# Performance work log

Measured on AMD Instinct MI355X. Metric: run time of the kernel, lower is better.

## Reference

```python
import jax, jax.numpy as jnp
import numpy as np

D_MODEL = 1024
NUM_HEADS = 16
HEAD_DIM = D_MODEL // NUM_HEADS


def setup_inputs() -> dict:
    key = jax.random.key(0)
    ks = jax.random.split(key, 10)
    B, SQ, SKV = 4, 2048, 2048
    s = 1.0 / np.sqrt(D_MODEL)
    return {
        "query": jax.random.normal(ks[0], (B, SQ, D_MODEL), jnp.float32),
        "key_value": jax.random.normal(ks[1], (B, SKV, D_MODEL), jnp.float32),
        "Wq": jax.random.normal(ks[2], (D_MODEL, D_MODEL), jnp.float32) * s,
        "bq": jnp.zeros((D_MODEL,), jnp.float32),
        "Wk": jax.random.normal(ks[3], (D_MODEL, D_MODEL), jnp.float32) * s,
        "bk": jnp.zeros((D_MODEL,), jnp.float32),
        "Wv": jax.random.normal(ks[4], (D_MODEL, D_MODEL), jnp.float32) * s,
        "bv": jnp.zeros((D_MODEL,), jnp.float32),
        "Wo": jax.random.normal(ks[5], (D_MODEL, D_MODEL), jnp.float32) * s,
        "bo": jnp.zeros((D_MODEL,), jnp.float32),
    }


def reference(query, key_value, Wq, bq, Wk, bk, Wv, bv, Wo, bo):
    B, SQ, _ = query.shape
    SKV = key_value.shape[1]
    H, Dh = NUM_HEADS, HEAD_DIM
    # projections (torch Linear: x @ W.T + b); split heads -> (B, H, S, Dh)
    Q = (query @ Wq.T + bq).reshape(B, SQ, H, Dh).transpose(0, 2, 1, 3)
    K = (key_value @ Wk.T + bk).reshape(B, SKV, H, Dh).transpose(0, 2, 1, 3)
    V = (key_value @ Wv.T + bv).reshape(B, SKV, H, Dh).transpose(0, 2, 1, 3)
    scale = jnp.asarray(np.sqrt(Dh), query.dtype)
    scores = jnp.einsum("bhqd,bhkd->bhqk", Q, K) / scale
    weights = jax.nn.softmax(scores, axis=-1)  # dropout is identity in eval
    attn = jnp.einsum("bhqk,bhkd->bhqd", weights, V)
    attn = attn.transpose(0, 2, 1, 3).reshape(B, SQ, H * Dh)
    return attn @ Wo.T + bo
```

## Files before the change

### kernel.cpp

```cpp
#include <hip/hip_runtime.h>

#define NH 16
#define DH 64
#define DM 1024
#define SEQ 2048
#define BATCH 4

typedef short s16x8 __attribute__((ext_vector_type(8)));
typedef float f32x4 __attribute__((ext_vector_type(4)));

__device__ __forceinline__ unsigned short f2bf(float f) {
  union { float f; unsigned int u; } v; v.f = f;
  unsigned int u = v.u;
  unsigned int r = (u + 0x7fffu + ((u >> 16) & 1u)) >> 16;
  return (unsigned short)r;
}

__device__ __forceinline__ unsigned int pkbf(float a, float b) {
#if __has_builtin(__builtin_amdgcn_cvt_pk_bf16_f32)
  typedef short v2s __attribute__((ext_vector_type(2)));
  v2s r = __builtin_amdgcn_cvt_pk_bf16_f32(a, b);
  union { v2s v; unsigned int u; } cv; cv.v = r;
  return cv.u;
#else
  return (unsigned int)f2bf(a) | ((unsigned int)f2bf(b) << 16);
#endif
}

__device__ __forceinline__ float fexp2(float x) {
#if __has_builtin(__builtin_amdgcn_exp2f)
  return __builtin_amdgcn_exp2f(x);
#else
  return exp2f(x);
#endif
}

__device__ __forceinline__ void gload_lds16(const void* g, void* l) {
  __builtin_amdgcn_global_load_lds(
      (const __attribute__((address_space(1))) unsigned int*)g,
      (__attribute__((address_space(3))) unsigned int*)l, 16, 0, 0);
}

__global__ void convert_all(const float* __restrict__ q, const float* __restrict__ kv,
                            const float* __restrict__ w0, const float* __restrict__ w1,
                            const float* __restrict__ w2, const float* __restrict__ w3,
                            unsigned short* __restrict__ oq, unsigned short* __restrict__ okv,
                            unsigned short* __restrict__ ow0, unsigned short* __restrict__ ow1,
                            unsigned short* __restrict__ ow2, unsigned short* __restrict__ ow3) {
  const int NQ4 = (BATCH * SEQ * DM) / 4;
  const int NW4 = (DM * DM) / 4;
  const int total = NQ4 * 2 + NW4 * 4;
  for (int i = blockIdx.x * blockDim.x + threadIdx.x; i < total;
       i += gridDim.x * blockDim.x) {
    const float* s; unsigned short* d; int off;
    if (i < NQ4)            { s = q;  d = oq;  off = i; }
    else if (i < 2 * NQ4)   { s = kv; d = okv; off = i - NQ4; }
    else {
      int j = i - 2 * NQ4; int wsel = j / NW4; off = j - wsel * NW4;
      s = (wsel == 0) ? w0 : (wsel == 1) ? w1 : (wsel == 2) ? w2 : w3;
      d = (wsel == 0) ? ow0 : (wsel == 1) ? ow1 : (wsel == 2) ? ow2 : ow3;
    }
    float4 v = *(const float4*)(s + (size_t)off * 4);
    ushort4 o;
    o.x = f2bf(v.x); o.y = f2bf(v.y); o.z = f2bf(v.z); o.w = f2bf(v.w);
    *(ushort4*)(d + (size_t)off * 4) = o;
  }
}

__device__ __forceinline__ void gemm_tile(const unsigned short* __restrict__ X,
                                          const unsigned short* __restrict__ Wt,
                                          unsigned short* As, unsigned short* Bs,
                                          int m0, int n0, f32x4 (*acc)[4]) {
  const int tid = threadIdx.x;
  const int wv_ = tid >> 6, lane = tid & 63;
  const int quad = lane >> 4, c = lane & 15;
  const int wm = (wv_ >> 1) * 64, wn = (wv_ & 1) * 64;
  const int srow = lane >> 3;
  const int scol = ((lane & 7) ^ srow) * 8;

  for (int kt = 0; kt < DM; kt += 64) {
#pragma unroll
    for (int i = 0; i < 4; ++i) {
      int reg = wv_ * 4 + i;
      gload_lds16(X + (size_t)(m0 + reg * 8 + srow) * DM + kt + scol,
                  (void*)(As + reg * 512));
      gload_lds16(Wt + (size_t)(n0 + reg * 8 + srow) * DM + kt + scol,
                  (void*)(Bs + reg * 512));
    }
    __syncthreads();
#pragma unroll
    for (int k2 = 0; k2 < 2; ++k2) {
      s16x8 a[4], b[4];
      int g = k2 * 4 + quad;
#pragma unroll
      for (int t = 0; t < 4; ++t)
        a[t] = *(const s16x8*)(As + (wm + t * 16 + c) * 64 + ((g ^ (c & 7)) * 8));
#pragma unroll
      for (int t = 0; t < 4; ++t)
        b[t] = *(const s16x8*)(Bs + (wn + t * 16 + c) * 64 + ((g ^ (c & 7)) * 8));
#pragma unroll
      for (int tm = 0; tm < 4; ++tm)
#pragma unroll
        for (int tn = 0; tn < 4; ++tn)
          acc[tm][tn] = __builtin_amdgcn_mfma_f32_16x16x32_bf16(
              a[tm], b[tn], acc[tm][tn], 0, 0, 0);
    }
    __syncthreads();
  }
}

__global__ __launch_bounds__(256)
void gemm_qkv(const unsigned short* __restrict__ Xq,
              const unsigned short* __restrict__ Xkv,
              const unsigned short* __restrict__ W0,
              const unsigned short* __restrict__ W1,
              const unsigned short* __restrict__ W2,
              const float* __restrict__ b0, const float* __restrict__ b1,
              const float* __restrict__ b2,
              unsigned short* __restrict__ OQ, unsigned short* __restrict__ OK_,
              unsigned short* __restrict__ OV) {
  __shared__ alignas(16) unsigned short As[128 * 64];
  __shared__ alignas(16) unsigned short Bs[128 * 64];
  const int m0 = blockIdx.x * 128;
  const int ysel = blockIdx.y >> 3;
  const int n0 = (blockIdx.y & 7) * 128;
  const unsigned short* X = (ysel == 0) ? Xq : Xkv;
  const unsigned short* Wt = (ysel == 0) ? W0 : (ysel == 1) ? W1 : W2;
  const float* bias = (ysel == 0) ? b0 : (ysel == 1) ? b1 : b2;
  unsigned short* Out = (ysel == 0) ? OQ : (ysel == 1) ? OK_ : OV;
  const float scale = (ysel == 0) ? 0.1803368801f : 1.0f;

  f32x4 acc[4][4] = {};
  gemm_tile(X, Wt, As, Bs, m0, n0, acc);

  const int tid = threadIdx.x;
  const int wv_ = tid >> 6, lane = tid & 63;
  const int quad = lane >> 4, c = lane & 15;
  const int wm = (wv_ >> 1) * 64, wn = (wv_ & 1) * 64;
#pragma unroll
  for (int tm = 0; tm < 4; ++tm) {
#pragma unroll
    for (int tn = 0; tn < 4; ++tn) {
      int n = n0 + wn + tn * 16 + c;
      float bv = bias[n];
      int m_base = m0 + wm + tm * 16 + quad * 4;
      if (ysel == 2) {
        int b_ = m_base >> 11, s_ = m_base & 2047, h_ = n >> 6, dh = n & 63;
        size_t idx = (((size_t)(b_ * NH + h_)) * DH + dh) * SEQ + s_;
        ushort4 o4;
        o4.x = f2bf(acc[tm][tn][0] + bv);
        o4.y = f2bf(acc[tm][tn][1] + bv);
        o4.z = f2bf(acc[tm][tn][2] + bv);
        o4.w = f2bf(acc[tm][tn][3] + bv);
        *(ushort4*)(&Out[idx]) = o4;
      } else {
#pragma unroll
        for (int p = 0; p < 4; ++p) {
          int m = m_base + p;
          float val = (acc[tm][tn][p] + bv) * scale;
          int b_ = m >> 11, s_ = m & 2047, h_ = n >> 6, dh = n & 63;
          size_t idx = (((size_t)(b_ * NH + h_)) * SEQ + s_) * DH + dh;
          Out[idx] = f2bf(val);
        }
      }
    }
  }
}

__global__ __launch_bounds__(256)
void gemm_o(const unsigned short* __restrict__ X,
            const unsigned short* __restrict__ Wt,
            const float* __restrict__ bias, float* __restrict__ Out) {
  __shared__ alignas(16) unsigned short As[128 * 64];
  __shared__ alignas(16) unsigned short Bs[128 * 64];
  const int m0 = blockIdx.x * 128;
  const int n0 = blockIdx.y * 128;
  f32x4 acc[4][4] = {};
  gemm_tile(X, Wt, As, Bs, m0, n0, acc);

  const int tid = threadIdx.x;
  const int wv_ = tid >> 6, lane = tid & 63;
  const int quad = lane >> 4, c = lane & 15;
  const int wm = (wv_ >> 1) * 64, wn = (wv_ & 1) * 64;
#pragma unroll
  for (int tm = 0; tm < 4; ++tm) {
#pragma unroll
    for (int tn = 0; tn < 4; ++tn) {
      int n = n0 + wn + tn * 16 + c;
      float bv = bias[n];
#pragma unroll
      for (int p = 0; p < 4; ++p) {
        int m = m0 + wm + tm * 16 + quad * 4 + p;
        Out[(size_t)m * DM + n] = acc[tm][tn][p] + bv;
      }
    }
  }
}

__global__ __launch_bounds__(512, 2)
void attn_kernel(const unsigned short* __restrict__ Qb,
                 const unsigned short* __restrict__ Kb,
                 const unsigned short* __restrict__ VTb,
                 unsigned short* __restrict__ Ob) {
  __shared__ alignas(16) unsigned short SM[18432];

  const int tid = threadIdx.x, wv_ = tid >> 6, lane = tid & 63;
  const int quad = lane >> 4, c = lane & 15;
  const int wg = blockIdx.x;
  const int bh = (wg & 7) + 8 * ((wg >> 3) >> 2);
  const int qb = (wg >> 3) & 3;
  const unsigned short* Qp = Qb + (size_t)bh * SEQ * DH;
  const unsigned short* Kp = Kb + (size_t)bh * SEQ * DH;
  const unsigned short* Vp = VTb + (size_t)bh * DH * SEQ;
  const int wq0 = qb * 512 + wv_ * 64;

  s16x8 aq[4][2];
#pragma unroll
  for (int t = 0; t < 4; ++t)
#pragma unroll
    for (int k2 = 0; k2 < 2; ++k2)
      aq[t][k2] = *(const s16x8*)(Qp + (size_t)(wq0 + t * 16 + c) * DH +
                                  k2 * 32 + quad * 8);

  f32x4 ot[4][4] = {};
  f32x4 lacc[4] = {};
  s16x8 ones;
  {
    union { s16x8 v; unsigned short u[8]; } o_;
#pragma unroll
    for (int j = 0; j < 8; ++j) o_.u[j] = 0x3F80;
    ones = o_.v;
  }

  const int srow = lane >> 3;
  const int sbase = (lane & 7) ^ (srow & 3);

  const int fK = (c & 3) | (((c >> 2) & 1) << 2);
  const int fV = (c & 3) | (((c >> 3) & 1) << 2);

#pragma unroll
  for (int i = 0; i < 2; ++i) {
    int slab = wv_ * 2 + i;
    if (slab < 8) {
      int ch = sbase ^ ((slab & 1) << 2);
      gload_lds16(Kp + (size_t)(slab * 8 + srow) * DH + ch * 8,
                  (void*)(SM + slab * 512));
    } else {
      int s2 = slab - 8;
      int ch = sbase ^ ((s2 & 1) << 2);
      gload_lds16(Vp + (size_t)(s2 * 8 + srow) * SEQ + ch * 8,
                  (void*)(SM + 8192 + s2 * 512));
    }
  }

  for (int kt = 0; kt < SEQ; kt += 64) {
    const int cur = (kt >> 6) & 1;
    __syncthreads();
    if (kt + 64 < SEQ) {
      const int nxt = cur ^ 1;
#pragma unroll
      for (int i = 0; i < 2; ++i) {
        int slab = wv_ * 2 + i;
        if (slab < 8) {
          int ch = sbase ^ ((slab & 1) << 2);
          gload_lds16(Kp + (size_t)(kt + 64 + slab * 8 + srow) * DH + ch * 8,
                      (void*)(SM + nxt * 4096 + slab * 512));
        } else {
          int s2 = slab - 8;
          int ch = sbase ^ ((s2 & 1) << 2);
          gload_lds16(Vp + (size_t)(s2 * 8 + srow) * SEQ + kt + 64 + ch * 8,
                      (void*)(SM + 8192 + nxt * 4096 + s2 * 512));
        }
      }
    }
    const unsigned short* K_ = SM + cur * 4096;
    const unsigned short* V_ = SM + 8192 + cur * 4096;

    f32x4 s[4][2][2] = {};
#pragma unroll
    for (int k2 = 0; k2 < 2; ++k2) {
      s16x8 ak[2][2];
#pragma unroll
      for (int jp = 0; jp < 2; ++jp)
#pragma unroll
        for (int h = 0; h < 2; ++h) {
          int r = jp * 32 + ((c >> 2) << 3) + h * 4 + (c & 3);
          int g = k2 * 4 + quad;
          ak[jp][h] = *(const s16x8*)(K_ + r * 64 + ((g ^ fK) * 8));
        }
#pragma unroll
      for (int t = 0; t < 4; ++t)
#pragma unroll
        for (int jp = 0; jp < 2; ++jp)
#pragma unroll
          for (int h = 0; h < 2; ++h)
            s[t][jp][h] = __builtin_amdgcn_mfma_f32_16x16x32_bf16(
                ak[jp][h], aq[t][k2], s[t][jp][h], 0, 0, 0);
    }

    s16x8 bp[4][2];
#pragma unroll
    for (int t = 0; t < 4; ++t)
#pragma unroll
      for (int jp = 0; jp < 2; ++jp) {
        float e00 = fexp2(s[t][jp][0][0]);
        float e01 = fexp2(s[t][jp][0][1]);
        float e02 = fexp2(s[t][jp][0][2]);
        float e03 = fexp2(s[t][jp][0][3]);
        float e10 = fexp2(s[t][jp][1][0]);
        float e11 = fexp2(s[t][jp][1][1]);
        float e12 = fexp2(s[t][jp][1][2]);
        float e13 = fexp2(s[t][jp][1][3]);
        union { s16x8 v; unsigned int u[4]; } pk;
        pk.u[0] = pkbf(e00, e01);
        pk.u[1] = pkbf(e02, e03);
        pk.u[2] = pkbf(e10, e11);
        pk.u[3] = pkbf(e12, e13);
        bp[t][jp] = pk.v;
        lacc[t] = __builtin_amdgcn_mfma_f32_16x16x32_bf16(
            ones, bp[t][jp], lacc[t], 0, 0, 0);
      }

#pragma unroll
    for (int jp = 0; jp < 2; ++jp)
#pragma unroll
      for (int dt = 0; dt < 4; ++dt) {
        int g = jp * 4 + quad;
        int r = dt * 16 + c;
        s16x8 av = *(const s16x8*)(V_ + r * 64 + ((g ^ fV) * 8));
#pragma unroll
        for (int t = 0; t < 4; ++t)
          ot[dt][t] = __builtin_amdgcn_mfma_f32_16x16x32_bf16(
              av, bp[t][jp], ot[dt][t], 0, 0, 0);
      }
  }

  __syncthreads();

  const int b_ = bh >> 4, h_ = bh & 15;
  const int ql = lane >> 1, hf = lane & 1;
  unsigned short* Lq = SM + wv_ * (32 * 72);
#pragma unroll
  for (int half = 0; half < 2; ++half) {
    if (half) asm volatile("s_waitcnt lgkmcnt(0)" ::: "memory");
#pragma unroll
    for (int t2 = 0; t2 < 2; ++t2) {
      int t = half * 2 + t2;
      float inv = 1.0f / lacc[t][0];
#pragma unroll
      for (int dt = 0; dt < 4; ++dt) {
        unsigned int w01 = pkbf(ot[dt][t][0] * inv, ot[dt][t][1] * inv);
        unsigned int w23 = pkbf(ot[dt][t][2] * inv, ot[dt][t][3] * inv);
        unsigned short* p = Lq + (t2 * 16 + c) * 72 + dt * 16 + quad * 4;
        *(unsigned int*)(p) = w01;
        *(unsigned int*)(p + 2) = w23;
      }
    }
    const unsigned short* Lr = Lq + ql * 72 + hf * 32;
    unsigned short* Og = Ob + ((size_t)(b_ * SEQ + wq0 + half * 32 + ql)) * DM +
                         h_ * 64 + hf * 32;
#pragma unroll
    for (int j = 0; j < 4; ++j) {
      s16x8 v = *(const s16x8*)(Lr + j * 8);
      *(s16x8*)(Og + j * 8) = v;
    }
  }
}

extern "C" void kernel_launch(void* const* d_in, const int* in_sizes, int n_in,
                              void* d_out, int out_size, void* d_ws, size_t ws_size,
                              hipStream_t stream) {
  const float* q  = (const float*)d_in[0];
  const float* kv = (const float*)d_in[1];
  const float* Wq = (const float*)d_in[2];
  const float* bq = (const float*)d_in[3];
  const float* Wk = (const float*)d_in[4];
  const float* bk = (const float*)d_in[5];
  const float* Wv = (const float*)d_in[6];
  const float* bv = (const float*)d_in[7];
  const float* Wo = (const float*)d_in[8];
  const float* bo = (const float*)d_in[9];

  char* ws = (char*)d_ws;
  const size_t MB = 1024 * 1024;
  unsigned short* q_bf  = (unsigned short*)(ws);
  unsigned short* kv_bf = (unsigned short*)(ws + 16 * MB);
  unsigned short* wq_bf = (unsigned short*)(ws + 32 * MB);
  unsigned short* wk_bf = (unsigned short*)(ws + 34 * MB);
  unsigned short* wv_bf = (unsigned short*)(ws + 36 * MB);
  unsigned short* wo_bf = (unsigned short*)(ws + 38 * MB);
  unsigned short* Qb    = (unsigned short*)(ws + 40 * MB);
  unsigned short* Kb    = (unsigned short*)(ws + 56 * MB);
  unsigned short* VTb   = (unsigned short*)(ws + 72 * MB);
  unsigned short* attn  = (unsigned short*)(ws + 88 * MB);

  convert_all<<<2048, 256, 0, stream>>>(q, kv, Wq, Wk, Wv, Wo,
                                        q_bf, kv_bf, wq_bf, wk_bf, wv_bf, wo_bf);
  gemm_qkv<<<dim3(64, 24), 256, 0, stream>>>(q_bf, kv_bf, wq_bf, wk_bf, wv_bf,
                                             bq, bk, bv, Qb, Kb, VTb);
  attn_kernel<<<dim3(256), 512, 0, stream>>>(Qb, Kb, VTb, attn);
  gemm_o<<<dim3(64, 8), 256, 0, stream>>>(attn, wo_bf, bo, (float*)d_out);
}
```

Baseline: 305.4 us.

## Stage 128-key tiles per barrier and raise MFMA wave priority in attention

The attention loop now stages K and V tiles of 128 keys per double-buffered step instead of 64, which halves the number of block barriers and makes each wave issue four async global-to-LDS loads per step. Each stage is processed as two 64-key halves. MFMA bursts are also wrapped in s_setprio so matrix work is favoured over other waves. Shared memory grows from about 36KB to 64KB per block, which could limit two blocks per CU under the launch bounds.

```diff
diff --git a/kernel.cpp b/kernel.cpp
--- a/kernel.cpp
+++ b/kernel.cpp
@@ -202,7 +202,7 @@
                  const unsigned short* __restrict__ Kb,
                  const unsigned short* __restrict__ VTb,
                  unsigned short* __restrict__ Ob) {
-  __shared__ alignas(16) unsigned short SM[18432];
+  __shared__ alignas(16) unsigned short SM[32768];
 
   const int tid = threadIdx.x, wv_ = tid >> 6, lane = tid & 63;
   const int quad = lane >> 4, c = lane & 15;
@@ -233,106 +233,97 @@
   }
 
   const int srow = lane >> 3;
-  const int sbase = (lane & 7) ^ (srow & 3);
+  const int ch = ((lane & 7) ^ (srow & 3)) ^ ((wv_ & 1) << 2);
 
   const int fK = (c & 3) | (((c >> 2) & 1) << 2);
   const int fV = (c & 3) | (((c >> 3) & 1) << 2);
 
-#pragma unroll
-  for (int i = 0; i < 2; ++i) {
-    int slab = wv_ * 2 + i;
-    if (slab < 8) {
-      int ch = sbase ^ ((slab & 1) << 2);
-      gload_lds16(Kp + (size_t)(slab * 8 + srow) * DH + ch * 8,
-                  (void*)(SM + slab * 512));
-    } else {
-      int s2 = slab - 8;
-      int ch = sbase ^ ((s2 & 1) << 2);
-      gload_lds16(Vp + (size_t)(s2 * 8 + srow) * SEQ + ch * 8,
-                  (void*)(SM + 8192 + s2 * 512));
-    }
-  }
-
-  for (int kt = 0; kt < SEQ; kt += 64) {
-    const int cur = (kt >> 6) & 1;
+#define STAGE_TILE(ktt, buf)                                                   \
+  {                                                                            \
+    gload_lds16(Kp + (size_t)((ktt) + wv_ * 8 + srow) * DH + ch * 8,           \
+                (void*)(SM + (buf) * 8192 + wv_ * 512));                       \
+    gload_lds16(Kp + (size_t)((ktt) + 64 + wv_ * 8 + srow) * DH + ch * 8,      \
+                (void*)(SM + (buf) * 8192 + 4096 + wv_ * 512));                \
+    gload_lds16(Vp + (size_t)(wv_ * 8 + srow) * SEQ + (ktt) + ch * 8,          \
+                (void*)(SM + 16384 + (buf) * 8192 + wv_ * 512));               \
+    gload_lds16(Vp + (size_t)(wv_ * 8 + srow) * SEQ + (ktt) + 64 + ch * 8,     \
+                (void*)(SM + 16384 + (buf) * 8192 + 4096 + wv_ * 512));        \
+  }
+
+  STAGE_TILE(0, 0);
+
+  for (int kt = 0; kt < SEQ; kt += 128) {
+    const int cur = (kt >> 7) & 1;
     __syncthreads();
-    if (kt + 64 < SEQ) {
-      const int nxt = cur ^ 1;
-#pragma unroll
-      for (int i = 0; i < 2; ++i) {
-        int slab = wv_ * 2 + i;
-        if (slab < 8) {
-          int ch = sbase ^ ((slab & 1) << 2);
-          gload_lds16(Kp + (size_t)(kt + 64 + slab * 8 + srow) * DH + ch * 8,
-                      (void*)(SM + nxt * 4096 + slab * 512));
-        } else {
-          int s2 = slab - 8;
-          int ch = sbase ^ ((s2 & 1) << 2);
-          gload_lds16(Vp + (size_t)(s2 * 8 + srow) * SEQ + kt + 64 + ch * 8,
-                      (void*)(SM + 8192 + nxt * 4096 + s2 * 512));
+    if (kt + 128 < SEQ) STAGE_TILE(kt + 128, cur ^ 1);
+
+#pragma unroll
+    for (int kh = 0; kh < 2; ++kh) {
+      const unsigned short* K_ = SM + cur * 8192 + kh * 4096;
+      const unsigned short* V_ = SM + 16384 + cur * 8192 + kh * 4096;
+
+      f32x4 s[4][2][2] = {};
+#pragma unroll
+      for (int k2 = 0; k2 < 2; ++k2) {
+        s16x8 ak[2][2];
+#pragma unroll
+        for (int jp = 0; jp < 2; ++jp)
+#pragma unroll
+          for (int h = 0; h < 2; ++h) {
+            int r = jp * 32 + ((c >> 2) << 3) + h * 4 + (c & 3);
+            int g = k2 * 4 + quad;
+            ak[jp][h] = *(const s16x8*)(K_ + r * 64 + ((g ^ fK) * 8));
+          }
+        __builtin_amdgcn_s_setprio(1);
+#pragma unroll
+        for (int t = 0; t < 4; ++t)
+#pragma unroll
+          for (int jp = 0; jp < 2; ++jp)
+#pragma unroll
+            for (int h = 0; h < 2; ++h)
+              s[t][jp][h] = __builtin_amdgcn_mfma_f32_16x16x32_bf16(
+                  ak[jp][h], aq[t][k2], s[t][jp][h], 0, 0, 0);
+        __builtin_amdgcn_s_setprio(0);
+      }
+
+      s16x8 bp[4][2];
+#pragma unroll
+      for (int t = 0; t < 4; ++t)
+#pragma unroll
+        for (int jp = 0; jp < 2; ++jp) {
+          float e00 = fexp2(s[t][jp][0][0]);
+          float e01 = fexp2(s[t][jp][0][1]);
+          float e02 = fexp2(s[t][jp][0][2]);
+          float e03 = fexp2(s[t][jp][0][3]);
+          float e10 = fexp2(s[t][jp][1][0]);
+          float e11 = fexp2(s[t][jp][1][1]);
+          float e12 = fexp2(s[t][jp][1][2]);
+          float e13 = fexp2(s[t][jp][1][3]);
+          union { s16x8 v; unsigned int u[4]; } pk;
+          pk.u[0] = pkbf(e00, e01);
+          pk.u[1] = pkbf(e02, e03);
+          pk.u[2] = pkbf(e10, e11);
+          pk.u[3] = pkbf(e12, e13);
+          bp[t][jp] = pk.v;
+          lacc[t] = __builtin_amdgcn_mfma_f32_16x16x32_bf16(
+              ones, bp[t][jp], lacc[t], 0, 0, 0);
         }
-      }
-    }
-    const unsigned short* K_ = SM + cur * 4096;
-    const unsigned short* V_ = SM + 8192 + cur * 4096;
-
-    f32x4 s[4][2][2] = {};
-#pragma unroll
-    for (int k2 = 0; k2 < 2; ++k2) {
-      s16x8 ak[2][2];
+
 #pragma unroll
       for (int jp = 0; jp < 2; ++jp)
 #pragma unroll
-        for (int h = 0; h < 2; ++h) {
-          int r = jp * 32 + ((c >> 2) << 3) + h * 4 + (c & 3);
-          int g = k2 * 4 + quad;
-          ak[jp][h] = *(const s16x8*)(K_ + r * 64 + ((g ^ fK) * 8));
+        for (int dt = 0; dt < 4; ++dt) {
+          int g = jp * 4 + quad;
+          int r = dt * 16 + c;
+          s16x8 av = *(const s16x8*)(V_ + r * 64 + ((g ^ fV) * 8));
+          __builtin_amdgcn_s_setprio(1);
+#pragma unroll
+          for (int t = 0; t < 4; ++t)
+            ot[dt][t] = __builtin_amdgcn_mfma_f32_16x16x32_bf16(
+                av, bp[t][jp], ot[dt][t], 0, 0, 0);
+          __builtin_amdgcn_s_setprio(0);
         }
-#pragma unroll
-      for (int t = 0; t < 4; ++t)
-#pragma unroll
-        for (int jp = 0; jp < 2; ++jp)
-#pragma unroll
-          for (int h = 0; h < 2; ++h)
-            s[t][jp][h] = __builtin_amdgcn_mfma_f32_16x16x32_bf16(
-                ak[jp][h], aq[t][k2], s[t][jp][h], 0, 0, 0);
-    }
-
-    s16x8 bp[4][2];
-#pragma unroll
-    for (int t = 0; t < 4; ++t)
-#pragma unroll
-      for (int jp = 0; jp < 2; ++jp) {
-        float e00 = fexp2(s[t][jp][0][0]);
-        float e01 = fexp2(s[t][jp][0][1]);
-        float e02 = fexp2(s[t][jp][0][2]);
-        float e03 = fexp2(s[t][jp][0][3]);
-        float e10 = fexp2(s[t][jp][1][0]);
-        float e11 = fexp2(s[t][jp][1][1]);
-        float e12 = fexp2(s[t][jp][1][2]);
-        float e13 = fexp2(s[t][jp][1][3]);
-        union { s16x8 v; unsigned int u[4]; } pk;
-        pk.u[0] = pkbf(e00, e01);
-        pk.u[1] = pkbf(e02, e03);
-        pk.u[2] = pkbf(e10, e11);
-        pk.u[3] = pkbf(e12, e13);
-        bp[t][jp] = pk.v;
-        lacc[t] = __builtin_amdgcn_mfma_f32_16x16x32_bf16(
-            ones, bp[t][jp], lacc[t], 0, 0, 0);
-      }
-
-#pragma unroll
-    for (int jp = 0; jp < 2; ++jp)
-#pragma unroll
-      for (int dt = 0; dt < 4; ++dt) {
-        int g = jp * 4 + quad;
-        int r = dt * 16 + c;
-        s16x8 av = *(const s16x8*)(V_ + r * 64 + ((g ^ fV) * 8));
-#pragma unroll
-        for (int t = 0; t < 4; ++t)
-          ot[dt][t] = __builtin_amdgcn_mfma_f32_16x16x32_bf16(
-              av, bp[t][jp], ot[dt][t], 0, 0, 0);
-      }
+    }
   }
 
   __syncthreads();
@@ -365,6 +356,7 @@
       *(s16x8*)(Og + j * 8) = v;
     }
   }
+#undef STAGE_TILE
 }
 
 extern "C" void kernel_launch(void* const* d_in, const int* in_sizes, int n_in,
```

Measured after the change: 304.9 us. About the same (-0.2%).
